# Kernel tuning notes

Measured on AMD Instinct MI355X. Metric: run time of the kernel, lower is better.

The kernel has to match this reference:

```python
import math
import jax, jax.numpy as jnp
import numpy as np

L, H = 4, 8  # num_layers, num_heads
SPARSE_FACTOR = 0.1
NEG = -1e9


def _ln(x, g, b, eps=1e-5):
    m = jnp.mean(x, axis=-1, keepdims=True)
    v = jnp.mean(jnp.square(x - m), axis=-1, keepdims=True)
    return (x - m) * jax.lax.rsqrt(v + eps) * g + b


def _pos_enc(S, D):
    # sinusoidal PE, shape (S, 1, D) matching pe.unsqueeze(0).transpose(0,1)[:S]
    pos = np.arange(S, dtype=np.float32)[:, None]
    div = np.exp(np.arange(0, D, 2, dtype=np.float32) * (-math.log(10000.0) / D))
    pe = np.zeros((S, D), dtype=np.float32)
    pe[:, 0::2] = np.sin(pos * div)
    pe[:, 1::2] = np.cos(pos * div)
    return jnp.asarray(pe)[:, None, :]


def setup_inputs() -> dict:
    key = jax.random.key(0)
    B, S, I, D, F = 128, 512, 64, 512, 2048
    ks = jax.random.split(key, 10)
    w = lambda k, shape: jax.random.normal(k, shape, jnp.float32) * 0.02
    return {
        'x': jax.random.normal(ks[0], (B, S, I), jnp.float32),
        'W_in': w(ks[1], (I, D)), 'b_in': jnp.zeros((D,), jnp.float32),
        'ln1_g': jnp.ones((L, D), jnp.float32), 'ln1_b': jnp.zeros((L, D), jnp.float32),
        'Wq': w(ks[2], (L, D, D)), 'Wk': w(ks[3], (L, D, D)), 'Wv': w(ks[4], (L, D, D)),
        'Wo': w(ks[5], (L, D, D)), 'bo': jnp.zeros((L, D), jnp.float32),
        'ln2_g': jnp.ones((L, D), jnp.float32), 'ln2_b': jnp.zeros((L, D), jnp.float32),
        'W1': w(ks[6], (L, D, F)), 'b1': jnp.zeros((L, F), jnp.float32),
        'W2': w(ks[7], (L, F, D)), 'b2': jnp.zeros((L, D), jnp.float32),
        'lnf_g': jnp.ones((D,), jnp.float32), 'lnf_b': jnp.zeros((D,), jnp.float32),
    }


def reference(x, W_in, b_in, ln1_g, ln1_b, Wq, Wk, Wv, Wo, bo,
              ln2_g, ln2_b, W1, b1, W2, b2, lnf_g, lnf_b):
    B, S, _ = x.shape
    D = W_in.shape[1]
    dk = D // H
    # source: scores last dim == batch (view+transpose quirk); k = max(1, int(B*0.1))
    topk = max(1, int(B * SPARSE_FACTOR))
    h = jnp.swapaxes(x, 0, 1) @ W_in + b_in          # (S,B,D)
    h = h * math.sqrt(D) + _pos_enc(S, D)

    def heads(z, w):
        return jnp.swapaxes((z @ w).reshape(S, B, H, dk), 1, 2)  # (S,H,B,dk)

    def body(h, p):
        g1, bb1, wq, wk, wv, wo, bo_, g2, bb2, w1, b1_, w2, b2_ = p
        y = _ln(h, g1, bb1)
        q, k, v = heads(y, wq), heads(y, wk), heads(y, wv)
        scores = jnp.einsum('shbd,shcd->shbc', q, k) / math.sqrt(dk)  # (S,H,B,B)
        kth = jax.lax.top_k(scores, topk)[0][..., -1:]
        scores = jnp.where(scores >= kth, scores, NEG)  # top-k sparsification
        attn = jax.nn.softmax(scores, axis=-1)
        ctx = jnp.einsum('shbc,shcd->shbd', attn, v)
        ctx = jnp.swapaxes(ctx, 1, 2).reshape(S, B, D)
        h = ctx @ wo + bo_ + h                       # attn out + residual
        f = jax.nn.gelu(_ln(h, g2, bb2) @ w1 + b1_, approximate=False) @ w2 + b2_
        return h + f, None

    h, _ = jax.lax.scan(body, h, (ln1_g, ln1_b, Wq, Wk, Wv, Wo, bo,
                                  ln2_g, ln2_b, W1, b1, W2, b2))
    h = _ln(h, lnf_g, lnf_b)
    return jnp.swapaxes(h, 0, 1)                     # (B,S,D)
```

## Files before the change

### kernel.cpp

```cpp
#include <hip/hip_runtime.h>
#include <math.h>

#define S_ 512
#define B_ 128
#define D_ 512
#define I_ 64
#define F_ 2048
#define H_ 8
#define DK_ 64
#define L_ 4
#define SB_ (S_*B_)

typedef unsigned short u16;
typedef unsigned int u32;
typedef __attribute__((ext_vector_type(4))) unsigned int u32x4;
typedef __attribute__((ext_vector_type(4))) float f32x4;

__device__ __forceinline__ u16 f2bf(float f){
  u32 x = __builtin_bit_cast(u32, f);
  x += 0x7fffu + ((x >> 16) & 1u);
  return (u16)(x >> 16);
}

__device__ __forceinline__ void mfma16(f32x4& c, const u32x4& a, const u32x4& b){
  asm volatile("v_mfma_f32_16x16x32_bf16 %0, %1, %2, %0" : "+v"(c) : "v"(a), "v"(b));
}

__device__ __forceinline__ void gload16(const u16* g, u16* l){
  __builtin_amdgcn_global_load_lds((const __attribute__((address_space(1))) unsigned int*)g,
                                   (__attribute__((address_space(3))) unsigned int*)l, 16, 0, 0);
}

__global__ void pe_kernel(float* __restrict__ pe){
  int s = blockIdx.x, d = threadIdx.x;
  float e = expf((float)(d & ~1) * (-9.210340371976184f / (float)D_));
  float arg = (float)s * e;
  pe[s*D_ + d] = (d & 1) ? cosf(arg) : sinf(arg);
}

__global__ void transpose_bf16(const float* __restrict__ src, u16* __restrict__ dst,
                               int R, int C, size_t zstride){
  __shared__ float t[32][33];
  size_t sbase = (size_t)blockIdx.z * R * C;
  size_t dbase = (size_t)blockIdx.z * zstride;
  int r0 = blockIdx.y*32, c0 = blockIdx.x*32;
  int tx = threadIdx.x, ty = threadIdx.y;
  #pragma unroll
  for (int j=0;j<4;j++)
    t[ty+j*8][tx] = src[sbase + (size_t)(r0+ty+j*8)*C + c0+tx];
  __syncthreads();
  #pragma unroll
  for (int j=0;j<4;j++)
    dst[dbase + (size_t)(c0+ty+j*8)*R + r0+tx] = f2bf(t[tx][ty+j*8]);
}

__global__ __launch_bounds__(512) void inproj_kernel(const float* __restrict__ x,
    const float* __restrict__ Win, const float* __restrict__ bin,
    const float* __restrict__ pe, float* __restrict__ h){
  __shared__ float xs[8][64];
  int t = threadIdx.x;
  float w[64];
  #pragma unroll
  for (int i=0;i<64;i++) w[i] = Win[i*D_ + t];
  float bd = bin[t];
  int r0 = blockIdx.x * 128;
  for (int batch=0; batch<16; batch++){
    int rb = r0 + batch*8;
    {
      int rr = t >> 6, i = t & 63;
      int r = rb + rr;
      int s = r >> 7, b = r & 127;
      xs[rr][i] = x[((size_t)b*S_ + s)*I_ + i];
    }
    __syncthreads();
    float acc[8];
    #pragma unroll
    for (int rr=0;rr<8;rr++) acc[rr] = 0.f;
    #pragma unroll
    for (int i4=0;i4<16;i4++){
      f32x4 xv[8];
      #pragma unroll
      for (int rr=0;rr<8;rr++) xv[rr] = *(const f32x4*)&xs[rr][i4*4];
      #pragma unroll
      for (int rr=0;rr<8;rr++){
        acc[rr] = fmaf(xv[rr][0], w[i4*4+0], acc[rr]);
        acc[rr] = fmaf(xv[rr][1], w[i4*4+1], acc[rr]);
        acc[rr] = fmaf(xv[rr][2], w[i4*4+2], acc[rr]);
        acc[rr] = fmaf(xv[rr][3], w[i4*4+3], acc[rr]);
      }
    }
    #pragma unroll
    for (int rr=0;rr<8;rr++){
      int r = rb + rr;
      int s = r >> 7;
      h[(size_t)r*D_ + t] = (acc[rr] + bd) * 22.627416997969522f + pe[s*D_ + t];
    }
    __syncthreads();
  }
}

template<int FINAL>
__global__ __launch_bounds__(256) void ln_kernel(const float* __restrict__ hsrc,
    const float* __restrict__ g, const float* __restrict__ bb,
    u16* __restrict__ outb, float* __restrict__ outf){
  int row = blockIdx.x*4 + (threadIdx.x>>6);
  int lane = threadIdx.x & 63;
  const float* hr = hsrc + (size_t)row*D_ + lane*8;
  f32x4 a0 = *(const f32x4*)hr;
  f32x4 a1 = *(const f32x4*)(hr+4);
  float v[8];
  #pragma unroll
  for (int j=0;j<4;j++){ v[j]=a0[j]; v[4+j]=a1[j]; }
  float sum = 0.f;
  #pragma unroll
  for (int j=0;j<8;j++) sum += v[j];
  #pragma unroll
  for (int m=1;m<64;m<<=1) sum += __shfl_xor(sum, m);
  float mean = sum * (1.f/(float)D_);
  float s2 = 0.f;
  #pragma unroll
  for (int j=0;j<8;j++){ float dd = v[j]-mean; s2 = fmaf(dd,dd,s2); }
  #pragma unroll
  for (int m=1;m<64;m<<=1) s2 += __shfl_xor(s2, m);
  float inv = rsqrtf(s2*(1.f/(float)D_) + 1e-5f);
  f32x4 g0 = *(const f32x4*)&g[lane*8];
  f32x4 g1 = *(const f32x4*)&g[lane*8+4];
  f32x4 b0 = *(const f32x4*)&bb[lane*8];
  f32x4 b1 = *(const f32x4*)&bb[lane*8+4];
  float o[8];
  #pragma unroll
  for (int j=0;j<4;j++){
    o[j]   = (v[j]-mean)*inv*g0[j] + b0[j];
    o[4+j] = (v[4+j]-mean)*inv*g1[j] + b1[j];
  }
  if (FINAL == 0){
    u32x4 pk;
    #pragma unroll
    for (int j=0;j<4;j++)
      pk[j] = (u32)f2bf(o[2*j]) | ((u32)f2bf(o[2*j+1])<<16);
    *(u32x4*)&outb[(size_t)row*D_ + lane*8] = pk;
  } else {
    int s = row>>7, b = row&(B_-1);
    float* op = outf + ((size_t)b*S_ + s)*D_ + lane*8;
    f32x4 r0, r1;
    #pragma unroll
    for (int j=0;j<4;j++){ r0[j]=o[j]; r1[j]=o[4+j]; }
    *(f32x4*)op = r0;
    *(f32x4*)(op+4) = r1;
  }
}

template<int MODE>
__global__ __launch_bounds__(256) void gemm_kernel(const u16* __restrict__ A,
    const u16* __restrict__ Wt, const float* __restrict__ bias,
    float* __restrict__ hres, u16* __restrict__ outb, int N, int K){
  const u32 nwg = gridDim.x * gridDim.y;
  u32 wg = blockIdx.y * gridDim.x + blockIdx.x;
  wg = (wg & 7) * (nwg >> 3) + (wg >> 3);
  const int m0 = (int)(wg / gridDim.x) * 128;
  const int n0 = (int)(wg % gridDim.x) * 128;
  __shared__ u16 a_lds[128*32];
  __shared__ u16 b_lds[128*32];
  const int t = threadIdx.x;
  const int lane = t & 63, wave = t >> 6;
  const int wm = wave >> 1, wn = wave & 1;
  const int rsel = lane & 15, kg = (lane>>4)*8;
  const u16* ag = A  + (size_t)(m0 + (t>>2))*K + (t&3)*8;
  const u16* bg = Wt + (size_t)(n0 + (t>>2))*K + (t&3)*8;
  f32x4 acc[4][4] = {};
  for (int k0 = 0; k0 < K; k0 += 32){
    asm volatile("s_nop 7\n\ts_nop 7");
    __syncthreads();
    gload16(ag + k0,                &a_lds[t*8]);
    gload16(ag + 64*(size_t)K + k0, &a_lds[2048 + t*8]);
    gload16(bg + k0,                &b_lds[t*8]);
    gload16(bg + 64*(size_t)K + k0, &b_lds[2048 + t*8]);
    __syncthreads();
    u32x4 af[4], bfr[4];
    #pragma unroll
    for (int i=0;i<4;i++){
      af[i]  = *(const u32x4*)&a_lds[(wm*64 + i*16 + rsel)*32 + kg];
      bfr[i] = *(const u32x4*)&b_lds[(wn*64 + i*16 + rsel)*32 + kg];
    }
    #pragma unroll
    for (int i=0;i<4;i++)
      #pragma unroll
      for (int j=0;j<4;j++)
        mfma16(acc[i][j], af[i], bfr[j]);
  }
  asm volatile("s_nop 7\n\ts_nop 7");
  const int rb = (lane>>4)*4;
  #pragma unroll
  for (int i=0;i<4;i++){
    #pragma unroll
    for (int j=0;j<4;j++){
      int gn = n0 + wn*64 + j*16 + rsel;
      #pragma unroll
      for (int rg=0;rg<4;rg++){
        int gr = m0 + wm*64 + i*16 + rb + rg;
        float val = acc[i][j][rg];
        if (MODE == 0){
          int mat = gn >> 9;
          int hh = (gn >> 6) & 7, dd = gn & 63;
          int s = gr >> 7, b = gr & 127;
          u16* dst = outb + (size_t)mat*33554432ull;
          dst[(size_t)((s*H_ + hh)*B_ + b)*DK_ + dd] = f2bf(val);
        } else if (MODE == 1){
          hres[(size_t)gr*D_ + gn] += val + bias[gn];
        } else {
          float xg = val + bias[gn];
          float ge = 0.5f*xg*(1.f + erff(xg*0.7071067811865476f));
          outb[(size_t)gr*(size_t)N + gn] = f2bf(ge);
        }
      }
    }
  }
}

__global__ __launch_bounds__(256, 2) void attn_kernel(const u16* __restrict__ qb,
    const u16* __restrict__ kb, const u16* __restrict__ vb, u16* __restrict__ cb){
  __shared__ __align__(16) char smem[79872];
  u16* q_lds = (u16*)smem;
  u16* k_lds = (u16*)(smem + 18432);
  float* S   = (float*)smem;
  u32* wl    = (u32*)(smem + 67584);
  int sh = blockIdx.x;
  int s = sh >> 3, hh = sh & 7;
  int t = threadIdx.x, lane = t & 63, wave = t >> 6;
  const u16* qg = qb + (size_t)sh * (B_*DK_);
  const u16* kg = kb + (size_t)sh * (B_*DK_);
  const u16* vg = vb + (size_t)sh * (B_*DK_);
  #pragma unroll
  for (int rr=0; rr<4; rr++){
    int idx = rr*2048 + t*8;
    int row = idx >> 6, col = idx & 63;
    *(u32x4*)&q_lds[row*72+col] = *(const u32x4*)&qg[idx];
    *(u32x4*)&k_lds[row*72+col] = *(const u32x4*)&kg[idx];
  }
  __syncthreads();
  int wm = wave>>1, wn = wave&1, rsel = lane & 15;
  f32x4 sacc[4][4] = {};
  #pragma unroll
  for (int ks=0; ks<2; ks++){
    asm volatile("s_nop 7\n\ts_nop 7");
    int ko = ks*32 + (lane>>4)*8;
    u32x4 qf[4], kf[4];
    #pragma unroll
    for (int i=0;i<4;i++){
      qf[i] = *(const u32x4*)&q_lds[(wm*64+i*16+rsel)*72 + ko];
      kf[i] = *(const u32x4*)&k_lds[(wn*64+i*16+rsel)*72 + ko];
    }
    #pragma unroll
    for (int i=0;i<4;i++)
      #pragma unroll
      for (int j=0;j<4;j++)
        mfma16(sacc[i][j], qf[i], kf[j]);
  }
  asm volatile("s_nop 7\n\ts_nop 7");
  __syncthreads();
  int rb = (lane>>4)*4;
  #pragma unroll
  for (int i=0;i<4;i++)
    #pragma unroll
    for (int j=0;j<4;j++)
      #pragma unroll
      for (int rg=0;rg<4;rg++)
        S[(wm*64+i*16+rb+rg)*132 + wn*64+j*16+rsel] = sacc[i][j][rg] * 0.125f;
  __syncthreads();
  int r = t >> 1, half = t & 1;
  const f32x4* srow4 = (const f32x4*)(S + r*132 + half*64);
  float kv[12];
  #pragma unroll
  for (int i=0;i<12;i++) kv[i] = -3.4e38f;
  for (int i4=0;i4<16;i4++){
    f32x4 v4 = srow4[i4];
    float m4 = fmaxf(fmaxf(v4[0],v4[1]), fmaxf(v4[2],v4[3]));
    if (m4 > kv[11]){
      #pragma unroll
      for (int z=0; z<4; z++){
        float inc = v4[z];
        if (inc > kv[11]){
          #pragma unroll
          for (int p=0;p<12;p++){
            float cur = kv[p];
            bool gt = inc > cur;
            kv[p] = gt ? inc : cur;
            inc   = gt ? cur : inc;
          }
        }
      }
    }
  }
  float kth = 3.4e38f;
  #pragma unroll
  for (int i=0;i<12;i++){
    float pb = __shfl_xor(kv[11-i], 1);
    kth = fminf(kth, fmaxf(kv[i], pb));
  }
  float mx = fmaxf(kv[0], __shfl_xor(kv[0], 1));
  float sum = 0.f;
  int n = 0;
  u32* myw = wl + t*12;
  for (int i4=0;i4<16;i4++){
    f32x4 v4 = srow4[i4];
    #pragma unroll
    for (int z=0; z<4; z++){
      float v = v4[z];
      if (v >= kth && n < 12){
        float e = __expf(v - mx);
        sum += e;
        myw[n] = ((u32)f2bf(e) << 16) | (u32)(half*64 + i4*4 + z);
        n++;
      }
    }
  }
  float tsum = sum + __shfl_xor(sum, 1);
  float facc[64];
  #pragma unroll
  for (int d=0; d<64; d++) facc[d] = 0.f;
  for (int j=0; j<n; j++){
    u32 e = myw[j];
    float w = __builtin_bit_cast(float, e & 0xffff0000u);
    const u32x4* vr = (const u32x4*)(vg + (size_t)(e & 0xffffu)*DK_);
    #pragma unroll
    for (int q8=0;q8<8;q8++){
      u32x4 u = vr[q8];
      #pragma unroll
      for (int z=0;z<4;z++){
        float lo = __builtin_bit_cast(float, u[z] << 16);
        float hi = __builtin_bit_cast(float, u[z] & 0xffff0000u);
        facc[q8*8+z*2]   = fmaf(w, lo, facc[q8*8+z*2]);
        facc[q8*8+z*2+1] = fmaf(w, hi, facc[q8*8+z*2+1]);
      }
    }
  }
  float inv = 1.f / tsum;
  u16* orow = cb + ((size_t)(s*B_ + r))*D_ + hh*DK_ + half*32;
  #pragma unroll
  for (int q4=0; q4<4; q4++){
    u32x4 pkk;
    #pragma unroll
    for (int z=0; z<2; z++){
      int d = q4*8 + z*4;
      float lo0 = facc[d]      + __shfl_xor(facc[d],      1);
      float lo1 = facc[d+1]    + __shfl_xor(facc[d+1],    1);
      float lo2 = facc[d+2]    + __shfl_xor(facc[d+2],    1);
      float lo3 = facc[d+3]    + __shfl_xor(facc[d+3],    1);
      float hi0 = facc[32+d]   + __shfl_xor(facc[32+d],   1);
      float hi1 = facc[32+d+1] + __shfl_xor(facc[32+d+1], 1);
      float hi2 = facc[32+d+2] + __shfl_xor(facc[32+d+2], 1);
      float hi3 = facc[32+d+3] + __shfl_xor(facc[32+d+3], 1);
      float o0 = (half ? hi0 : lo0) * inv;
      float o1 = (half ? hi1 : lo1) * inv;
      float o2 = (half ? hi2 : lo2) * inv;
      float o3 = (half ? hi3 : lo3) * inv;
      pkk[z*2]   = (u32)f2bf(o0) | ((u32)f2bf(o1) << 16);
      pkk[z*2+1] = (u32)f2bf(o2) | ((u32)f2bf(o3) << 16);
    }
    *(u32x4*)(orow + q4*8) = pkk;
  }
}

extern "C" void kernel_launch(void* const* d_in, const int* in_sizes, int n_in,
                              void* d_out, int out_size, void* d_ws, size_t ws_size,
                              hipStream_t stream) {
  const float* x    = (const float*)d_in[0];
  const float* Win  = (const float*)d_in[1];
  const float* bin  = (const float*)d_in[2];
  const float* ln1g = (const float*)d_in[3];
  const float* ln1b = (const float*)d_in[4];
  const float* Wq   = (const float*)d_in[5];
  const float* Wk   = (const float*)d_in[6];
  const float* Wv   = (const float*)d_in[7];
  const float* Wo   = (const float*)d_in[8];
  const float* bo   = (const float*)d_in[9];
  const float* ln2g = (const float*)d_in[10];
  const float* ln2b = (const float*)d_in[11];
  const float* W1   = (const float*)d_in[12];
  const float* b1   = (const float*)d_in[13];
  const float* W2   = (const float*)d_in[14];
  const float* b2   = (const float*)d_in[15];
  const float* lnfg = (const float*)d_in[16];
  const float* lnfb = (const float*)d_in[17];

  char* ws = (char*)d_ws;
  float* h  = (float*)(ws);
  u16* yb   = (u16*)(ws + 134217728ull);
  u16* qb   = (u16*)(ws + 201326592ull);
  u16* kb   = (u16*)(ws + 268435456ull);
  u16* vb   = (u16*)(ws + 335544320ull);
  u16* cb   = (u16*)(ws + 402653184ull);
  u16* act  = qb;
  u16* wqkvT= (u16*)(ws + 469762048ull);
  u16* woT  = (u16*)(ws + 476053504ull);
  u16* w1T  = (u16*)(ws + 478150656ull);
  u16* w2T  = (u16*)(ws + 486539264ull);
  float* pe = (float*)(ws + 494927872ull);

  dim3 tb(32,8);
  pe_kernel<<<S_, D_, 0, stream>>>(pe);
  transpose_bf16<<<dim3(D_/32, D_/32, L_), tb, 0, stream>>>(Wq, wqkvT,            D_, D_, (size_t)3*D_*D_);
  transpose_bf16<<<dim3(D_/32, D_/32, L_), tb, 0, stream>>>(Wk, wqkvT + D_*D_,    D_, D_, (size_t)3*D_*D_);
  transpose_bf16<<<dim3(D_/32, D_/32, L_), tb, 0, stream>>>(Wv, wqkvT + 2*D_*D_,  D_, D_, (size_t)3*D_*D_);
  transpose_bf16<<<dim3(D_/32, D_/32, L_), tb, 0, stream>>>(Wo, woT,              D_, D_, (size_t)D_*D_);
  transpose_bf16<<<dim3(F_/32, D_/32, L_), tb, 0, stream>>>(W1, w1T, D_, F_, (size_t)D_*F_);
  transpose_bf16<<<dim3(D_/32, F_/32, L_), tb, 0, stream>>>(W2, w2T, F_, D_, (size_t)F_*D_);
  inproj_kernel<<<512, 512, 0, stream>>>(x, Win, bin, pe, h);

  for (int l=0; l<L_; l++){
    ln_kernel<0><<<SB_/4, 256, 0, stream>>>(h, ln1g + l*D_, ln1b + l*D_, yb, nullptr);
    gemm_kernel<0><<<dim3(12,512), 256, 0, stream>>>(yb, wqkvT + (size_t)l*3*D_*D_, nullptr, nullptr, qb, 1536, D_);
    attn_kernel<<<S_*H_, 256, 0, stream>>>(qb, kb, vb, cb);
    gemm_kernel<1><<<dim3(4,512), 256, 0, stream>>>(cb, woT + (size_t)l*D_*D_, bo + l*D_, h, nullptr, D_, D_);
    ln_kernel<0><<<SB_/4, 256, 0, stream>>>(h, ln2g + l*D_, ln2b + l*D_, yb, nullptr);
    gemm_kernel<2><<<dim3(16,512), 256, 0, stream>>>(yb, w1T + (size_t)l*D_*F_, b1 + l*F_, nullptr, act, F_, D_);
    gemm_kernel<1><<<dim3(4,512), 256, 0, stream>>>(act, w2T + (size_t)l*F_*D_, b2 + l*D_, h, nullptr, D_, F_);
  }
  ln_kernel<1><<<SB_/4, 256, 0, stream>>>(h, lnfg, lnfb, nullptr, (float*)d_out);
}
```

Measured before the change: 3.858 ms.

## Compute attention P·V with MFMA on a dense LDS probability matrix

```diff
diff --git a/kernel.cpp b/kernel.cpp
--- a/kernel.cpp
+++ b/kernel.cpp
@@ -219,11 +219,14 @@
 
 __global__ __launch_bounds__(256, 2) void attn_kernel(const u16* __restrict__ qb,
     const u16* __restrict__ kb, const u16* __restrict__ vb, u16* __restrict__ cb){
-  __shared__ __align__(16) char smem[79872];
+  __shared__ __align__(16) char smem[80384];
   u16* q_lds = (u16*)smem;
   u16* k_lds = (u16*)(smem + 18432);
   float* S   = (float*)smem;
+  u16* P     = (u16*)smem;
+  u16* vT    = (u16*)(smem + 34816);
   u32* wl    = (u32*)(smem + 67584);
+  float* rs  = (float*)(smem + 79872);
   int sh = blockIdx.x;
   int s = sh >> 3, hh = sh & 7;
   int t = threadIdx.x, lane = t & 63, wave = t >> 6;
@@ -315,50 +318,59 @@
     }
   }
   float tsum = sum + __shfl_xor(sum, 1);
-  float facc[64];
-  #pragma unroll
-  for (int d=0; d<64; d++) facc[d] = 0.f;
+  if (!half) rs[r] = 1.f / tsum;
+  __syncthreads();
+  {
+    u32x4 zz = {0u,0u,0u,0u};
+    #pragma unroll
+    for (int z=0; z<9; z++){
+      int idx = z*256 + t;
+      if (idx < 2176) ((u32x4*)P)[idx] = zz;
+    }
+  }
+  #pragma unroll
+  for (int rr=0; rr<16; rr++){
+    int idx2 = (rr*256 + t)*2;
+    u32 u = *(const u32*)&vg[idx2];
+    int c = idx2 >> 6, d0 = idx2 & 63;
+    vT[d0*136 + c]     = (u16)(u & 0xffffu);
+    vT[(d0+1)*136 + c] = (u16)(u >> 16);
+  }
+  __syncthreads();
+  u16* prow = P + r*136;
   for (int j=0; j<n; j++){
     u32 e = myw[j];
-    float w = __builtin_bit_cast(float, e & 0xffff0000u);
-    const u32x4* vr = (const u32x4*)(vg + (size_t)(e & 0xffffu)*DK_);
-    #pragma unroll
-    for (int q8=0;q8<8;q8++){
-      u32x4 u = vr[q8];
-      #pragma unroll
-      for (int z=0;z<4;z++){
-        float lo = __builtin_bit_cast(float, u[z] << 16);
-        float hi = __builtin_bit_cast(float, u[z] & 0xffff0000u);
-        facc[q8*8+z*2]   = fmaf(w, lo, facc[q8*8+z*2]);
-        facc[q8*8+z*2+1] = fmaf(w, hi, facc[q8*8+z*2+1]);
+    prow[e & 0xffffu] = (u16)(e >> 16);
+  }
+  __syncthreads();
+  f32x4 cacc[4][2] = {};
+  #pragma unroll
+  for (int ks=0; ks<4; ks++){
+    asm volatile("s_nop 7\n\ts_nop 7");
+    int ko = ks*32 + (lane>>4)*8;
+    u32x4 pf[4], vf[2];
+    #pragma unroll
+    for (int i=0;i<4;i++) pf[i] = *(const u32x4*)&P[(wm*64+i*16+rsel)*136 + ko];
+    #pragma unroll
+    for (int j=0;j<2;j++) vf[j] = *(const u32x4*)&vT[(wn*32+j*16+rsel)*136 + ko];
+    #pragma unroll
+    for (int i=0;i<4;i++)
+      #pragma unroll
+      for (int j=0;j<2;j++)
+        mfma16(cacc[i][j], pf[i], vf[j]);
+  }
+  asm volatile("s_nop 7\n\ts_nop 7");
+  #pragma unroll
+  for (int i=0;i<4;i++)
+    #pragma unroll
+    for (int j=0;j<2;j++)
+      #pragma unroll
+      for (int rg=0;rg<4;rg++){
+        int m = wm*64 + i*16 + rb + rg;
+        int nn = wn*32 + j*16 + rsel;
+        float val = cacc[i][j][rg] * rs[m];
+        cb[((size_t)(s*B_ + m))*D_ + hh*DK_ + nn] = f2bf(val);
       }
-    }
-  }
-  float inv = 1.f / tsum;
-  u16* orow = cb + ((size_t)(s*B_ + r))*D_ + hh*DK_ + half*32;
-  #pragma unroll
-  for (int q4=0; q4<4; q4++){
-    u32x4 pkk;
-    #pragma unroll
-    for (int z=0; z<2; z++){
-      int d = q4*8 + z*4;
-      float lo0 = facc[d]      + __shfl_xor(facc[d],      1);
-      float lo1 = facc[d+1]    + __shfl_xor(facc[d+1],    1);
-      float lo2 = facc[d+2]    + __shfl_xor(facc[d+2],    1);
-      float lo3 = facc[d+3]    + __shfl_xor(facc[d+3],    1);
-      float hi0 = facc[32+d]   + __shfl_xor(facc[32+d],   1);
-      float hi1 = facc[32+d+1] + __shfl_xor(facc[32+d+1], 1);
-      float hi2 = facc[32+d+2] + __shfl_xor(facc[32+d+2], 1);
-      float hi3 = facc[32+d+3] + __shfl_xor(facc[32+d+3], 1);
-      float o0 = (half ? hi0 : lo0) * inv;
-      float o1 = (half ? hi1 : lo1) * inv;
-      float o2 = (half ? hi2 : lo2) * inv;
-      float o3 = (half ? hi3 : lo3) * inv;
-      pkk[z*2]   = (u32)f2bf(o0) | ((u32)f2bf(o1) << 16);
-      pkk[z*2+1] = (u32)f2bf(o2) | ((u32)f2bf(o3) << 16);
-    }
-    *(u32x4*)(orow + q4*8) = pkk;
-  }
 }
 
 extern "C" void kernel_launch(void* const* d_in, const int* in_sizes, int n_in,
```

Result: faster. 3.664 ms (-5.0%).
